# Kernel optimization log

Measured on AMD Instinct MI355X. Metric: run time of the kernel, lower is better.

## Reference

```python
import jax, jax.numpy as jnp
import numpy as np

N_NODES = 100000
N_EDGES = 1600000
N_GRAPHS = 512
F_IN, HID, EMB = 256, 64, 2


def gcn_layer(h, src, dst, W, b, n_nodes):
    # PyG GCNConv: h' = D^{-1/2} (A + I) D^{-1/2} (h W) + b
    h = h @ W  # [N, out]
    loop = jnp.arange(n_nodes)
    s = jnp.concatenate([src, loop])
    d = jnp.concatenate([dst, loop])
    deg = jax.ops.segment_sum(jnp.ones_like(d, dtype=h.dtype), d, num_segments=n_nodes)
    dinv = jnp.where(deg > 0, jax.lax.rsqrt(deg), 0.0)
    norm = dinv[s] * dinv[d]  # [E+N]
    msg = h[s] * norm[:, None]  # gather + scale
    return jax.ops.segment_sum(msg, d, num_segments=n_nodes) + b


def setup_inputs() -> dict:
    key = jax.random.key(0)
    k1, k2, k3, k4, k5, k6 = jax.random.split(key, 6)
    x = jax.random.normal(k1, (N_NODES, F_IN), dtype=jnp.float32)
    edge_index = jax.random.randint(k2, (2, N_EDGES), 0, N_NODES, dtype=jnp.int64)
    batch = jnp.sort(jax.random.randint(k3, (N_NODES,), 0, N_GRAPHS, dtype=jnp.int64))
    # Glorot-ish init for layer weights
    W1 = jax.random.normal(k4, (F_IN, HID), dtype=jnp.float32) / np.sqrt(F_IN)
    b1 = jnp.zeros((HID,), dtype=jnp.float32)
    W2 = jax.random.normal(k5, (HID, EMB), dtype=jnp.float32) / np.sqrt(HID)
    b2 = jnp.zeros((EMB,), dtype=jnp.float32)
    return {"x": x, "edge_index": edge_index, "batch": batch,
            "W1": W1, "b1": b1, "W2": W2, "b2": b2}


def reference(x, edge_index, batch, W1, b1, W2, b2):
    n = x.shape[0]
    src, dst = edge_index[0], edge_index[1]
    h = gcn_layer(x, src, dst, W1, b1, n)
    h = jax.nn.relu(h)
    h = gcn_layer(h, src, dst, W2, b2, n)
    # global_mean_pool over graph ids
    sums = jax.ops.segment_sum(h, batch, num_segments=N_GRAPHS)
    cnts = jax.ops.segment_sum(jnp.ones((n,), dtype=h.dtype), batch, num_segments=N_GRAPHS)
    return sums / jnp.maximum(cnts, 1.0)[:, None]
```

## Files before the change

kernel.cpp:

```cpp
#include <hip/hip_runtime.h>
#include <hip/hip_bf16.h>

#define FIN 256
#define HID 64
#define EMB 2
#define BKB 9
#define BKSZ 512
#define MAXBK 256
#define NBLK 256

typedef __bf16 bf16x8 __attribute__((ext_vector_type(8)));
typedef float  f32x16 __attribute__((ext_vector_type(16)));

static __device__ __forceinline__ unsigned short f2bf(float f) {
    union { float f; unsigned int u; } v; v.f = f;
    unsigned int u = v.u;
    unsigned int r = (u + 0x7fffu + ((u >> 16) & 1u)) >> 16;
    return (unsigned short)r;
}
static __device__ __forceinline__ float bf2f(unsigned short h) {
    union { unsigned int u; float f; } v; v.u = ((unsigned int)h) << 16;
    return v.f;
}

__global__ __launch_bounds__(256) void bin_hist_kernel(
        const int* __restrict__ dst, int* __restrict__ counts, int E, int chunk, int NBK) {
    __shared__ int hist[MAXBK];
    int tid = threadIdx.x;
    for (int b = tid; b < NBK; b += 256) hist[b] = 0;
    __syncthreads();
    int e0 = blockIdx.x * chunk, e1 = min(e0 + chunk, E);
    for (int i = e0 + tid; i < e1; i += 256) atomicAdd(&hist[dst[i] >> BKB], 1);
    __syncthreads();
    for (int b = tid; b < NBK; b += 256) counts[b * gridDim.x + blockIdx.x] = hist[b];
}

__global__ __launch_bounds__(256) void scan_local_kernel(
        int* __restrict__ counts, int* __restrict__ btot) {
    __shared__ int s[256];
    const int b = blockIdx.x, tid = threadIdx.x;
    int v = counts[b * NBLK + tid];
    s[tid] = v;
    __syncthreads();
    for (int off = 1; off < 256; off <<= 1) {
        int t = (tid >= off) ? s[tid - off] : 0;
        __syncthreads();
        s[tid] += t;
        __syncthreads();
    }
    counts[b * NBLK + tid] = s[tid] - v;
    if (tid == 255) btot[b] = s[255];
}

__global__ __launch_bounds__(256) void scan_tot_kernel(
        const int* __restrict__ btot, int* __restrict__ bucketBase,
        float* __restrict__ sums, int NBK, int nzero) {
    __shared__ int s[256];
    const int tid = threadIdx.x;
    int v = (tid < NBK) ? btot[tid] : 0;
    s[tid] = v;
    __syncthreads();
    for (int off = 1; off < 256; off <<= 1) {
        int t = (tid >= off) ? s[tid - off] : 0;
        __syncthreads();
        s[tid] += t;
        __syncthreads();
    }
    if (tid < NBK) bucketBase[tid] = s[tid] - v;
    if (tid == NBK - 1) bucketBase[NBK] = s[tid];
    for (int i = tid; i < nzero; i += 256) sums[i] = 0.f;
}

__global__ __launch_bounds__(256) void bin_scatter_kernel(
        const int* __restrict__ src, const int* __restrict__ dst,
        const int* __restrict__ counts, const int* __restrict__ bucketBase,
        unsigned* __restrict__ ebuf, int E, int chunk, int NBK) {
    __shared__ int cur[MAXBK];
    int tid = threadIdx.x;
    for (int b = tid; b < NBK; b += 256)
        cur[b] = bucketBase[b] + counts[b * gridDim.x + blockIdx.x];
    __syncthreads();
    int e0 = blockIdx.x * chunk, e1 = min(e0 + chunk, E);
    for (int i = e0 + tid; i < e1; i += 256) {
        int s = src[i], d = dst[i];
        int b = d >> BKB;
        int pos = atomicAdd(&cur[b], 1);
        ebuf[pos] = ((unsigned)s << BKB) | (unsigned)(d & (BKSZ - 1));
    }
}

__global__ __launch_bounds__(256) void build_kernel(
        const unsigned* __restrict__ ebuf, const int* __restrict__ bucketBase,
        int* __restrict__ rowptr, float* __restrict__ dinv, int* __restrict__ csr,
        int N, int E) {
    __shared__ int hist[BKSZ];
    __shared__ int scanb[256];
    __shared__ int cur[BKSZ];
    const int b = blockIdx.x, tid = threadIdx.x;
    const int r0 = bucketBase[b];
    const int r1 = bucketBase[b + 1];
    const int nb0 = b * BKSZ;

    hist[tid] = 0; hist[tid + 256] = 0;
    __syncthreads();
    for (int i = r0 + tid; i < r1; i += 256)
        atomicAdd(&hist[ebuf[i] & (BKSZ - 1u)], 1);
    __syncthreads();

    int h0 = hist[2 * tid], h1 = hist[2 * tid + 1];
    if (nb0 + 2 * tid < N)     dinv[nb0 + 2 * tid]     = rsqrtf((float)h0 + 1.f);
    if (nb0 + 2 * tid + 1 < N) dinv[nb0 + 2 * tid + 1] = rsqrtf((float)h1 + 1.f);
    scanb[tid] = h0 + h1;
    __syncthreads();
    for (int off = 1; off < 256; off <<= 1) {
        int t = (tid >= off) ? scanb[tid - off] : 0;
        __syncthreads();
        scanb[tid] += t;
        __syncthreads();
    }
    int base0 = scanb[tid] - (h0 + h1);
    int o0 = base0, o1 = base0 + h0;
    cur[2 * tid] = o0; cur[2 * tid + 1] = o1;
    if (nb0 + 2 * tid < N)     rowptr[nb0 + 2 * tid]     = r0 + o0;
    if (nb0 + 2 * tid + 1 < N) rowptr[nb0 + 2 * tid + 1] = r0 + o1;
    if (nb0 + BKSZ >= N && tid == 0) rowptr[N] = E;
    __syncthreads();
    for (int i = r0 + tid; i < r1; i += 256) {
        unsigned u = ebuf[i];
        int loc = (int)(u & (BKSZ - 1u));
        int p = atomicAdd(&cur[loc], 1);
        csr[r0 + p] = (int)(u >> BKB);
    }
}

__global__ __launch_bounds__(256) void gemm1_kernel(
        const float* __restrict__ x, const float* __restrict__ W,
        const float* __restrict__ dinv, unsigned short* __restrict__ h1b, int N) {
    __shared__ __align__(16) __bf16 A_hi[2 * 4 * 64 * 8];
    __shared__ __align__(16) __bf16 A_lo[2 * 4 * 64 * 8];
    __shared__ __align__(16) __bf16 B_hi[2 * 4 * 64 * 8];
    __shared__ __align__(16) __bf16 B_lo[2 * 4 * 64 * 8];

    const int tid = threadIdx.x;
    const int base = blockIdx.x * 64;
    const int w = tid >> 6;
    const int l = tid & 63;
    const int mg = w >> 1, ng = w & 1;

    f32x16 acc = {};

    const int r  = tid & 63;
    const int ks = tid >> 6;
    const int rl = r & 31, rh = r >> 5;

    for (int ch = 0; ch < 4; ++ch) {
        const int ck0 = ch * 64;
        __syncthreads();
        {
            int row = base + r;
            float f[16];
            if (row < N) {
                const float* xp = &x[(size_t)row * FIN + ck0 + ks * 16];
                float4 v0 = *(const float4*)(xp + 0);
                float4 v1 = *(const float4*)(xp + 4);
                float4 v2 = *(const float4*)(xp + 8);
                float4 v3 = *(const float4*)(xp + 12);
                f[0]=v0.x; f[1]=v0.y; f[2]=v0.z; f[3]=v0.w;
                f[4]=v1.x; f[5]=v1.y; f[6]=v1.z; f[7]=v1.w;
                f[8]=v2.x; f[9]=v2.y; f[10]=v2.z; f[11]=v2.w;
                f[12]=v3.x; f[13]=v3.y; f[14]=v3.z; f[15]=v3.w;
            } else {
                #pragma unroll
                for (int q = 0; q < 16; ++q) f[q] = 0.f;
            }
            bf16x8 ha, hb, la, lb;
            #pragma unroll
            for (int q = 0; q < 8; ++q) {
                __bf16 h0 = (__bf16)f[q];
                ha[q] = h0; la[q] = (__bf16)(f[q] - (float)h0);
                __bf16 h1v = (__bf16)f[q + 8];
                hb[q] = h1v; lb[q] = (__bf16)(f[q + 8] - (float)h1v);
            }
            int ra = ((rh * 4 + ks) * 64 + rl) * 8;
            int rb = ((rh * 4 + ks) * 64 + 32 + rl) * 8;
            *(bf16x8*)&A_hi[ra] = ha; *(bf16x8*)&A_hi[rb] = hb;
            *(bf16x8*)&A_lo[ra] = la; *(bf16x8*)&A_lo[rb] = lb;
        }
        {
            const float* wp = &W[(size_t)(ck0 + ks * 16) * HID + r];
            float f[16];
            #pragma unroll
            for (int q = 0; q < 16; ++q) f[q] = wp[q * HID];
            bf16x8 ha, hb, la, lb;
            #pragma unroll
            for (int q = 0; q < 8; ++q) {
                __bf16 h0 = (__bf16)f[q];
                ha[q] = h0; la[q] = (__bf16)(f[q] - (float)h0);
                __bf16 h1v = (__bf16)f[q + 8];
                hb[q] = h1v; lb[q] = (__bf16)(f[q + 8] - (float)h1v);
            }
            int ra = ((rh * 4 + ks) * 64 + rl) * 8;
            int rb = ((rh * 4 + ks) * 64 + 32 + rl) * 8;
            *(bf16x8*)&B_hi[ra] = ha; *(bf16x8*)&B_hi[rb] = hb;
            *(bf16x8*)&B_lo[ra] = la; *(bf16x8*)&B_lo[rb] = lb;
        }
        __syncthreads();

        #pragma unroll
        for (int s = 0; s < 4; ++s) {
            bf16x8 a_h = *(const bf16x8*)&A_hi[((mg * 4 + s) * 64 + l) * 8];
            bf16x8 a_l = *(const bf16x8*)&A_lo[((mg * 4 + s) * 64 + l) * 8];
            bf16x8 b_h = *(const bf16x8*)&B_hi[((ng * 4 + s) * 64 + l) * 8];
            bf16x8 b_l = *(const bf16x8*)&B_lo[((ng * 4 + s) * 64 + l) * 8];
            acc = __builtin_amdgcn_mfma_f32_32x32x16_bf16(a_h, b_h, acc, 0, 0, 0);
            acc = __builtin_amdgcn_mfma_f32_32x32x16_bf16(a_h, b_l, acc, 0, 0, 0);
            acc = __builtin_amdgcn_mfma_f32_32x32x16_bf16(a_l, b_h, acc, 0, 0, 0);
        }
    }

    const int col = l & 31;
    const int rbase = 4 * (l >> 5);
    #pragma unroll
    for (int reg = 0; reg < 16; ++reg) {
        int row = (reg & 3) + 8 * (reg >> 2) + rbase;
        int node = base + mg * 32 + row;
        if (node < N)
            h1b[(size_t)node * HID + ng * 32 + col] = f2bf(acc[reg] * dinv[node]);
    }
}

__global__ __launch_bounds__(256) void agg1_layer2_kernel(
        const int* __restrict__ rowptr, const int* __restrict__ csr,
        const unsigned short* __restrict__ h1b,
        const float* __restrict__ dinv, const float* __restrict__ b1,
        const float* __restrict__ W2, float* __restrict__ h2, int N) {
    long t = (long)blockIdx.x * blockDim.x + threadIdx.x;
    int n = (int)(t >> 4);
    int li = threadIdx.x & 15;
    if (n >= N) return;
    const ushort4* h14 = (const ushort4*)h1b;

    float di = dinv[n];
    ushort4 sl = h14[(size_t)n * 16 + li];
    float v0 = bf2f(sl.x), v1 = bf2f(sl.y);
    float v2 = bf2f(sl.z), v3 = bf2f(sl.w);

    int j0 = rowptr[n], j1 = rowptr[n + 1];
    int j = j0;
    for (; j + 3 < j1; j += 4) {
        int s0 = csr[j], s1 = csr[j + 1], s2 = csr[j + 2], s3 = csr[j + 3];
        ushort4 g0 = h14[(size_t)s0 * 16 + li];
        ushort4 g1 = h14[(size_t)s1 * 16 + li];
        ushort4 g2 = h14[(size_t)s2 * 16 + li];
        ushort4 g3 = h14[(size_t)s3 * 16 + li];
        v0 += bf2f(g0.x) + bf2f(g1.x) + bf2f(g2.x) + bf2f(g3.x);
        v1 += bf2f(g0.y) + bf2f(g1.y) + bf2f(g2.y) + bf2f(g3.y);
        v2 += bf2f(g0.z) + bf2f(g1.z) + bf2f(g2.z) + bf2f(g3.z);
        v3 += bf2f(g0.w) + bf2f(g1.w) + bf2f(g2.w) + bf2f(g3.w);
    }
    for (; j < j1; ++j) {
        int s = csr[j];
        ushort4 g = h14[(size_t)s * 16 + li];
        v0 += bf2f(g.x); v1 += bf2f(g.y); v2 += bf2f(g.z); v3 += bf2f(g.w);
    }

    const float4 b4 = *(const float4*)&b1[li * 4];
    v0 = fmaxf(di * v0 + b4.x, 0.f); v1 = fmaxf(di * v1 + b4.y, 0.f);
    v2 = fmaxf(di * v2 + b4.z, 0.f); v3 = fmaxf(di * v3 + b4.w, 0.f);

    const float4* W24 = (const float4*)W2;
    float4 wa = W24[li * 2], wb = W24[li * 2 + 1];
    float r0 = v0 * wa.x + v1 * wa.z + v2 * wb.x + v3 * wb.z;
    float r1 = v0 * wa.y + v1 * wa.w + v2 * wb.y + v3 * wb.w;
    #pragma unroll
    for (int off = 1; off < 16; off <<= 1) {
        r0 += __shfl_xor(r0, off);
        r1 += __shfl_xor(r1, off);
    }
    if (li == 0) *(float2*)&h2[(size_t)n * EMB] = make_float2(r0 * di, r1 * di);
}

__global__ __launch_bounds__(256) void agg2_pool_kernel(
        const int* __restrict__ rowptr, const int* __restrict__ csr,
        const float* __restrict__ h2,
        const float* __restrict__ dinv, const float* __restrict__ b2,
        const int* __restrict__ batch,
        float* __restrict__ sums, float* __restrict__ cntf, int N) {
    int n = blockIdx.x * blockDim.x + threadIdx.x;
    int lane = threadIdx.x & 63;
    const float2* h2v = (const float2*)h2;
    float v0 = 0.f, v1 = 0.f, c = 0.f;
    int g = -1;
    if (n < N) {
        float di = dinv[n];
        float2 hs = h2v[n];
        v0 = hs.x; v1 = hs.y;
        int j0 = rowptr[n], j1 = rowptr[n + 1];
        int j = j0;
        for (; j + 3 < j1; j += 4) {
            int s0 = csr[j], s1 = csr[j + 1], s2 = csr[j + 2], s3 = csr[j + 3];
            float2 a = h2v[s0], b = h2v[s1], cc = h2v[s2], d = h2v[s3];
            v0 += a.x + b.x + cc.x + d.x;
            v1 += a.y + b.y + cc.y + d.y;
        }
        for (; j < j1; ++j) {
            float2 hv = h2v[csr[j]];
            v0 += hv.x; v1 += hv.y;
        }
        v0 = di * v0 + b2[0];
        v1 = di * v1 + b2[1];
        g = batch[n];
        c = 1.f;
    }
    #pragma unroll
    for (int off = 1; off < 64; off <<= 1) {
        int gg = __shfl_up(g, off);
        float t0 = __shfl_up(v0, off);
        float t1 = __shfl_up(v1, off);
        float tc = __shfl_up(c, off);
        if (lane >= off && gg == g) { v0 += t0; v1 += t1; c += tc; }
    }
    int gn = __shfl_down(g, 1);
    if (g >= 0 && (lane == 63 || gn != g)) {
        atomicAdd(&sums[g * EMB + 0], v0);
        atomicAdd(&sums[g * EMB + 1], v1);
        atomicAdd(&cntf[g], c);
    }
}

__global__ void final_kernel(const float* __restrict__ sums, const float* __restrict__ cntf,
                             float* __restrict__ out, int G) {
    int g = blockIdx.x * blockDim.x + threadIdx.x;
    if (g >= G) return;
    float c = fmaxf(cntf[g], 1.0f);
    out[g * EMB + 0] = sums[g * EMB + 0] / c;
    out[g * EMB + 1] = sums[g * EMB + 1] / c;
}

extern "C" void kernel_launch(void* const* d_in, const int* in_sizes, int n_in,
                              void* d_out, int out_size, void* d_ws, size_t ws_size,
                              hipStream_t stream) {
    const float* x     = (const float*)d_in[0];
    const int*   ei    = (const int*)d_in[1];
    const int*   batch = (const int*)d_in[2];
    const float* W1    = (const float*)d_in[3];
    const float* b1    = (const float*)d_in[4];
    const float* W2    = (const float*)d_in[5];
    const float* b2    = (const float*)d_in[6];
    float* out = (float*)d_out;

    const int N = in_sizes[0] / FIN;
    const int E = in_sizes[1] / 2;
    const int G = out_size / EMB;
    const int* src = ei;
    const int* dst = ei + E;

    const int NBK = (N + BKSZ - 1) / BKSZ;
    const int chunk = (E + NBLK - 1) / NBLK;

    char* p = (char*)d_ws;
    auto take = [&](size_t bytes) { char* r = p; p += (bytes + 15) & ~(size_t)15; return r; };
    int*      counts = (int*)take(sizeof(int) * NBK * NBLK);
    int*      btot   = (int*)take(sizeof(int) * NBK);
    int*      bucketBase = (int*)take(sizeof(int) * (NBK + 1));
    unsigned* ebuf   = (unsigned*)take(sizeof(unsigned) * E);
    int*      csr    = (int*)take(sizeof(int) * E);
    int*      rowptr = (int*)take(sizeof(int) * (N + 1));
    float*    dinv   = (float*)take(sizeof(float) * N);
    unsigned short* h1b = (unsigned short*)take(sizeof(unsigned short) * (size_t)N * HID);
    float*    h2     = (float*)take(sizeof(float) * (size_t)N * EMB);
    float*    sums   = (float*)take(sizeof(float) * G * EMB);
    float*    cntf   = (float*)take(sizeof(float) * G);

    bin_hist_kernel<<<NBLK, 256, 0, stream>>>(dst, counts, E, chunk, NBK);
    scan_local_kernel<<<NBK, 256, 0, stream>>>(counts, btot);
    scan_tot_kernel<<<1, 256, 0, stream>>>(btot, bucketBase, sums, NBK, 3 * G);
    bin_scatter_kernel<<<NBLK, 256, 0, stream>>>(src, dst, counts, bucketBase, ebuf, E, chunk, NBK);
    build_kernel<<<NBK, 256, 0, stream>>>(ebuf, bucketBase, rowptr, dinv, csr, N, E);
    gemm1_kernel<<<(N + 63) / 64, 256, 0, stream>>>(x, W1, dinv, h1b, N);
    agg1_layer2_kernel<<<(int)(((long)N * 16 + 255) / 256), 256, 0, stream>>>(
        rowptr, csr, h1b, dinv, b1, W2, h2, N);
    agg2_pool_kernel<<<(N + 255) / 256, 256, 0, stream>>>(
        rowptr, csr, h2, dinv, b2, batch, sums, cntf, N);
    final_kernel<<<(G + 255) / 256, 256, 0, stream>>>(sums, cntf, out, G);
}
```

Baseline: 296.5 us.

## Merge CSR build kernels into one cooperative kernel and fuse final pooling

```diff
diff --git a/kernel.cpp b/kernel.cpp
--- a/kernel.cpp
+++ b/kernel.cpp
@@ -1,5 +1,8 @@
 #include <hip/hip_runtime.h>
 #include <hip/hip_bf16.h>
+#include <hip/hip_cooperative_groups.h>
+
+namespace cg = cooperative_groups;
 
 #define FIN 256
 #define HID 64
@@ -23,113 +26,115 @@
     return v.f;
 }
 
-__global__ __launch_bounds__(256) void bin_hist_kernel(
-        const int* __restrict__ dst, int* __restrict__ counts, int E, int chunk, int NBK) {
-    __shared__ int hist[MAXBK];
-    int tid = threadIdx.x;
-    for (int b = tid; b < NBK; b += 256) hist[b] = 0;
-    __syncthreads();
-    int e0 = blockIdx.x * chunk, e1 = min(e0 + chunk, E);
-    for (int i = e0 + tid; i < e1; i += 256) atomicAdd(&hist[dst[i] >> BKB], 1);
-    __syncthreads();
-    for (int b = tid; b < NBK; b += 256) counts[b * gridDim.x + blockIdx.x] = hist[b];
-}
-
-__global__ __launch_bounds__(256) void scan_local_kernel(
-        int* __restrict__ counts, int* __restrict__ btot) {
-    __shared__ int s[256];
-    const int b = blockIdx.x, tid = threadIdx.x;
-    int v = counts[b * NBLK + tid];
-    s[tid] = v;
-    __syncthreads();
-    for (int off = 1; off < 256; off <<= 1) {
-        int t = (tid >= off) ? s[tid - off] : 0;
-        __syncthreads();
-        s[tid] += t;
-        __syncthreads();
-    }
-    counts[b * NBLK + tid] = s[tid] - v;
-    if (tid == 255) btot[b] = s[255];
-}
-
-__global__ __launch_bounds__(256) void scan_tot_kernel(
-        const int* __restrict__ btot, int* __restrict__ bucketBase,
-        float* __restrict__ sums, int NBK, int nzero) {
-    __shared__ int s[256];
-    const int tid = threadIdx.x;
-    int v = (tid < NBK) ? btot[tid] : 0;
-    s[tid] = v;
-    __syncthreads();
-    for (int off = 1; off < 256; off <<= 1) {
-        int t = (tid >= off) ? s[tid - off] : 0;
-        __syncthreads();
-        s[tid] += t;
-        __syncthreads();
-    }
-    if (tid < NBK) bucketBase[tid] = s[tid] - v;
-    if (tid == NBK - 1) bucketBase[NBK] = s[tid];
-    for (int i = tid; i < nzero; i += 256) sums[i] = 0.f;
-}
-
-__global__ __launch_bounds__(256) void bin_scatter_kernel(
+__global__ __launch_bounds__(256) void build_all_kernel(
         const int* __restrict__ src, const int* __restrict__ dst,
-        const int* __restrict__ counts, const int* __restrict__ bucketBase,
-        unsigned* __restrict__ ebuf, int E, int chunk, int NBK) {
-    __shared__ int cur[MAXBK];
-    int tid = threadIdx.x;
-    for (int b = tid; b < NBK; b += 256)
-        cur[b] = bucketBase[b] + counts[b * gridDim.x + blockIdx.x];
-    __syncthreads();
-    int e0 = blockIdx.x * chunk, e1 = min(e0 + chunk, E);
-    for (int i = e0 + tid; i < e1; i += 256) {
-        int s = src[i], d = dst[i];
-        int b = d >> BKB;
-        int pos = atomicAdd(&cur[b], 1);
-        ebuf[pos] = ((unsigned)s << BKB) | (unsigned)(d & (BKSZ - 1));
-    }
-}
-
-__global__ __launch_bounds__(256) void build_kernel(
-        const unsigned* __restrict__ ebuf, const int* __restrict__ bucketBase,
+        int* __restrict__ counts, int* __restrict__ btot,
+        int* __restrict__ bucketBase, unsigned* __restrict__ ebuf,
         int* __restrict__ rowptr, float* __restrict__ dinv, int* __restrict__ csr,
-        int N, int E) {
-    __shared__ int hist[BKSZ];
-    __shared__ int scanb[256];
-    __shared__ int cur[BKSZ];
-    const int b = blockIdx.x, tid = threadIdx.x;
-    const int r0 = bucketBase[b];
-    const int r1 = bucketBase[b + 1];
-    const int nb0 = b * BKSZ;
-
-    hist[tid] = 0; hist[tid + 256] = 0;
-    __syncthreads();
-    for (int i = r0 + tid; i < r1; i += 256)
-        atomicAdd(&hist[ebuf[i] & (BKSZ - 1u)], 1);
-    __syncthreads();
-
-    int h0 = hist[2 * tid], h1 = hist[2 * tid + 1];
-    if (nb0 + 2 * tid < N)     dinv[nb0 + 2 * tid]     = rsqrtf((float)h0 + 1.f);
-    if (nb0 + 2 * tid + 1 < N) dinv[nb0 + 2 * tid + 1] = rsqrtf((float)h1 + 1.f);
-    scanb[tid] = h0 + h1;
-    __syncthreads();
-    for (int off = 1; off < 256; off <<= 1) {
-        int t = (tid >= off) ? scanb[tid - off] : 0;
-        __syncthreads();
-        scanb[tid] += t;
-        __syncthreads();
-    }
-    int base0 = scanb[tid] - (h0 + h1);
-    int o0 = base0, o1 = base0 + h0;
-    cur[2 * tid] = o0; cur[2 * tid + 1] = o1;
-    if (nb0 + 2 * tid < N)     rowptr[nb0 + 2 * tid]     = r0 + o0;
-    if (nb0 + 2 * tid + 1 < N) rowptr[nb0 + 2 * tid + 1] = r0 + o1;
-    if (nb0 + BKSZ >= N && tid == 0) rowptr[N] = E;
-    __syncthreads();
-    for (int i = r0 + tid; i < r1; i += 256) {
-        unsigned u = ebuf[i];
-        int loc = (int)(u & (BKSZ - 1u));
-        int p = atomicAdd(&cur[loc], 1);
-        csr[r0 + p] = (int)(u >> BKB);
+        float* __restrict__ sums, int* __restrict__ done,
+        int E, int chunk, int NBK, int N, int nzero) {
+    cg::grid_group grid = cg::this_grid();
+    __shared__ int lds[1280];
+    const int blk = blockIdx.x, tid = threadIdx.x;
+
+    {
+        int* hist = lds;
+        for (int b = tid; b < NBK; b += 256) hist[b] = 0;
+        __syncthreads();
+        int e0 = blk * chunk, e1 = min(e0 + chunk, E);
+        for (int i = e0 + tid; i < e1; i += 256) atomicAdd(&hist[dst[i] >> BKB], 1);
+        __syncthreads();
+        for (int b = tid; b < NBK; b += 256) counts[b * NBLK + blk] = hist[b];
+    }
+    grid.sync();
+
+    if (blk < NBK) {
+        int* s = lds;
+        int v = counts[blk * NBLK + tid];
+        s[tid] = v;
+        __syncthreads();
+        for (int off = 1; off < 256; off <<= 1) {
+            int t = (tid >= off) ? s[tid - off] : 0;
+            __syncthreads();
+            s[tid] += t;
+            __syncthreads();
+        }
+        counts[blk * NBLK + tid] = s[tid] - v;
+        if (tid == 255) btot[blk] = s[255];
+    }
+    grid.sync();
+
+    if (blk == 0) {
+        int* s = lds;
+        int v = (tid < NBK) ? btot[tid] : 0;
+        s[tid] = v;
+        __syncthreads();
+        for (int off = 1; off < 256; off <<= 1) {
+            int t = (tid >= off) ? s[tid - off] : 0;
+            __syncthreads();
+            s[tid] += t;
+            __syncthreads();
+        }
+        if (tid < NBK) bucketBase[tid] = s[tid] - v;
+        if (tid == NBK - 1) bucketBase[NBK] = s[tid];
+        for (int i = tid; i < nzero; i += 256) sums[i] = 0.f;
+        if (tid == 0) *done = 0;
+    }
+    grid.sync();
+
+    {
+        int* cur = lds;
+        for (int b = tid; b < NBK; b += 256)
+            cur[b] = bucketBase[b] + counts[b * NBLK + blk];
+        __syncthreads();
+        int e0 = blk * chunk, e1 = min(e0 + chunk, E);
+        for (int i = e0 + tid; i < e1; i += 256) {
+            int s = src[i], d = dst[i];
+            int b = d >> BKB;
+            int pos = atomicAdd(&cur[b], 1);
+            ebuf[pos] = ((unsigned)s << BKB) | (unsigned)(d & (BKSZ - 1));
+        }
+    }
+    grid.sync();
+
+    if (blk < NBK) {
+        int* hist  = lds;
+        int* scanb = lds + 512;
+        int* cur   = lds + 768;
+        const int r0 = bucketBase[blk];
+        const int r1 = bucketBase[blk + 1];
+        const int nb0 = blk * BKSZ;
+
+        hist[tid] = 0; hist[tid + 256] = 0;
+        __syncthreads();
+        for (int i = r0 + tid; i < r1; i += 256)
+            atomicAdd(&hist[ebuf[i] & (BKSZ - 1u)], 1);
+        __syncthreads();
+
+        int h0 = hist[2 * tid], h1 = hist[2 * tid + 1];
+        if (nb0 + 2 * tid < N)     dinv[nb0 + 2 * tid]     = rsqrtf((float)h0 + 1.f);
+        if (nb0 + 2 * tid + 1 < N) dinv[nb0 + 2 * tid + 1] = rsqrtf((float)h1 + 1.f);
+        scanb[tid] = h0 + h1;
+        __syncthreads();
+        for (int off = 1; off < 256; off <<= 1) {
+            int t = (tid >= off) ? scanb[tid - off] : 0;
+            __syncthreads();
+            scanb[tid] += t;
+            __syncthreads();
+        }
+        int base0 = scanb[tid] - (h0 + h1);
+        int o0 = base0, o1 = base0 + h0;
+        cur[2 * tid] = o0; cur[2 * tid + 1] = o1;
+        if (nb0 + 2 * tid < N)     rowptr[nb0 + 2 * tid]     = r0 + o0;
+        if (nb0 + 2 * tid + 1 < N) rowptr[nb0 + 2 * tid + 1] = r0 + o1;
+        if (nb0 + BKSZ >= N && tid == 0) rowptr[N] = E;
+        __syncthreads();
+        for (int i = r0 + tid; i < r1; i += 256) {
+            unsigned u = ebuf[i];
+            int loc = (int)(u & (BKSZ - 1u));
+            int p = atomicAdd(&cur[loc], 1);
+            csr[r0 + p] = (int)(u >> BKB);
+        }
     }
 }
 
@@ -280,12 +285,13 @@
     if (li == 0) *(float2*)&h2[(size_t)n * EMB] = make_float2(r0 * di, r1 * di);
 }
 
-__global__ __launch_bounds__(256) void agg2_pool_kernel(
+__global__ __launch_bounds__(256) void agg2_pool_final_kernel(
         const int* __restrict__ rowptr, const int* __restrict__ csr,
         const float* __restrict__ h2,
         const float* __restrict__ dinv, const float* __restrict__ b2,
         const int* __restrict__ batch,
-        float* __restrict__ sums, float* __restrict__ cntf, int N) {
+        float* __restrict__ sums, float* __restrict__ cntf,
+        float* __restrict__ out, int* __restrict__ done, int N, int G) {
     int n = blockIdx.x * blockDim.x + threadIdx.x;
     int lane = threadIdx.x & 63;
     const float2* h2v = (const float2*)h2;
@@ -326,15 +332,25 @@
         atomicAdd(&sums[g * EMB + 1], v1);
         atomicAdd(&cntf[g], c);
     }
-}
-
-__global__ void final_kernel(const float* __restrict__ sums, const float* __restrict__ cntf,
-                             float* __restrict__ out, int G) {
-    int g = blockIdx.x * blockDim.x + threadIdx.x;
-    if (g >= G) return;
-    float c = fmaxf(cntf[g], 1.0f);
-    out[g * EMB + 0] = sums[g * EMB + 0] / c;
-    out[g * EMB + 1] = sums[g * EMB + 1] / c;
+
+    __shared__ int isLast;
+    __threadfence();
+    if (threadIdx.x == 0) {
+        int v = atomicAdd(done, 1);
+        isLast = (v == (int)gridDim.x - 1);
+    }
+    __syncthreads();
+    if (isLast) {
+        __threadfence();
+        const volatile float* vs = sums;
+        const volatile float* vc = cntf;
+        for (int gg = threadIdx.x; gg < G; gg += blockDim.x) {
+            float cc = vc[gg];
+            cc = fmaxf(cc, 1.0f);
+            out[gg * EMB + 0] = vs[gg * EMB + 0] / cc;
+            out[gg * EMB + 1] = vs[gg * EMB + 1] / cc;
+        }
+    }
 }
 
 extern "C" void kernel_launch(void* const* d_in, const int* in_sizes, int n_in,
@@ -371,16 +387,21 @@
     float*    h2     = (float*)take(sizeof(float) * (size_t)N * EMB);
     float*    sums   = (float*)take(sizeof(float) * G * EMB);
     float*    cntf   = (float*)take(sizeof(float) * G);
-
-    bin_hist_kernel<<<NBLK, 256, 0, stream>>>(dst, counts, E, chunk, NBK);
-    scan_local_kernel<<<NBK, 256, 0, stream>>>(counts, btot);
-    scan_tot_kernel<<<1, 256, 0, stream>>>(btot, bucketBase, sums, NBK, 3 * G);
-    bin_scatter_kernel<<<NBLK, 256, 0, stream>>>(src, dst, counts, bucketBase, ebuf, E, chunk, NBK);
-    build_kernel<<<NBK, 256, 0, stream>>>(ebuf, bucketBase, rowptr, dinv, csr, N, E);
+    int*      done   = (int*)take(sizeof(int));
+
+    {
+        int E_ = E, chunk_ = chunk, NBK_ = NBK, N_ = N, nzero_ = 3 * G;
+        const int* src_ = src; const int* dst_ = dst;
+        void* args[] = { (void*)&src_, (void*)&dst_, (void*)&counts, (void*)&btot,
+                         (void*)&bucketBase, (void*)&ebuf, (void*)&rowptr, (void*)&dinv,
+                         (void*)&csr, (void*)&sums, (void*)&done,
+                         (void*)&E_, (void*)&chunk_, (void*)&NBK_, (void*)&N_, (void*)&nzero_ };
+        hipLaunchCooperativeKernel((void*)build_all_kernel, dim3(NBLK), dim3(256),
+                                   args, 0, stream);
+    }
     gemm1_kernel<<<(N + 63) / 64, 256, 0, stream>>>(x, W1, dinv, h1b, N);
     agg1_layer2_kernel<<<(int)(((long)N * 16 + 255) / 256), 256, 0, stream>>>(
         rowptr, csr, h1b, dinv, b1, W2, h2, N);
-    agg2_pool_kernel<<<(N + 255) / 256, 256, 0, stream>>>(
-        rowptr, csr, h2, dinv, b2, batch, sums, cntf, N);
-    final_kernel<<<(G + 255) / 256, 256, 0, stream>>>(sums, cntf, out, G);
-}
+    agg2_pool_final_kernel<<<(N + 255) / 256, 256, 0, stream>>>(
+        rowptr, csr, h2, dinv, b2, batch, sums, cntf, out, done, N, G);
+}
```

Result: slower. 453.0 us (+52.8%).
